# Kernel tuning notes

Measured on AMD Instinct MI355X. Metric: run time of the kernel, lower is better.

The kernel has to match this reference:

```python
import jax, jax.numpy as jnp
import numpy as np

RANK = 4
ALPHA = 32
SCALING = ALPHA / RANK  # 8.0
LORA_STRENGTH = 1.0


def setup_inputs() -> dict:
    key = jax.random.key(0)
    ks = jax.random.split(key, 7)
    d_out, d_in = 4096, 4096  # Mistral q/k/v/o_proj weight shape
    batch, seq = 1, 512
    x = jax.random.normal(ks[0], (batch, seq, d_in), dtype=jnp.float32)
    W = jax.random.normal(ks[1], (d_out, d_in), dtype=jnp.float32) * 0.02  # frozen base weight
    A = jax.random.normal(ks[2], (d_out, RANK), dtype=jnp.float32)
    B = jax.random.normal(ks[3], (RANK, d_in), dtype=jnp.float32)
    zc_w = jax.random.normal(ks[4], (), dtype=jnp.float32)  # Conv2d(1,1,1) weight (scalar)
    zc_b = jax.random.normal(ks[5], (), dtype=jnp.float32)  # Conv2d(1,1,1) bias (scalar)
    bias = jax.random.normal(ks[6], (d_out,), dtype=jnp.float32)
    return {"x": x, "W": W, "A": A, "B": B, "zc_w": zc_w, "zc_b": zc_b, "bias": bias}


def reference(x, W, A, B, zc_w, zc_b, bias):
    # low_rank_update = scaling * (A @ B), then 1x1 zero-conv = elementwise scale + bias
    low = SCALING * jnp.einsum('or,ri->oi', A, B)          # [d_out, d_in]
    low = zc_w * low + zc_b                                 # zero_conv (scalar affine)
    W_prime = LORA_STRENGTH * W + low                       # [d_out, d_in]
    # x @ W_prime.T + bias
    return jnp.einsum('bsi,oi->bso', x, W_prime) + bias
```

## Files before the change

### kernel.cpp

```cpp
#include <hip/hip_runtime.h>
#include <hip/hip_bf16.h>


typedef __attribute__((ext_vector_type(8))) short bf16x8;
typedef __attribute__((ext_vector_type(4))) short bf16x4;
typedef __attribute__((ext_vector_type(4))) unsigned short u16x4;
typedef __attribute__((ext_vector_type(4))) float f32x4;

#define MDIM 512
#define NDIM 4096
#define KDIM 4096
#define BM 128
#define BN 128
#define BK 64
#define NT (KDIM / BK)

#define VMCNT(n) asm volatile("s_waitcnt vmcnt(" #n ")" ::: "memory")
#define LGKM0()  asm volatile("s_waitcnt lgkmcnt(0)" ::: "memory")
#define SCHED0() __builtin_amdgcn_sched_barrier(0)

static __device__ inline unsigned short f2bf(float f) {
  return __bfloat16_as_ushort(__float2bfloat16(f));
}

static __device__ inline bf16x8 pack8(f32x4 a, f32x4 b) {
  bf16x8 v;
  v[0] = (short)f2bf(a[0]); v[1] = (short)f2bf(a[1]);
  v[2] = (short)f2bf(a[2]); v[3] = (short)f2bf(a[3]);
  v[4] = (short)f2bf(b[0]); v[5] = (short)f2bf(b[1]);
  v[6] = (short)f2bf(b[2]); v[7] = (short)f2bf(b[3]);
  return v;
}

static __device__ inline void gll16(const void* g, void* l) {
  __builtin_amdgcn_global_load_lds(
      (const __attribute__((address_space(1))) void*)g,
      (__attribute__((address_space(3))) void*)l, 16, 0, 0);
}

__global__ __launch_bounds__(256) void tk_kernel(
    const float* __restrict__ x, const float* __restrict__ B,
    float* __restrict__ t, float* __restrict__ xs,
    unsigned short* __restrict__ xbf) {
  const int tid = threadIdx.x;
  const int s = blockIdx.x;
  const float* xr = x + (long)s * KDIM;
  float a0 = 0.f, a1 = 0.f, a2 = 0.f, a3 = 0.f, a4 = 0.f;
  for (int k = tid * 4; k < KDIM; k += 1024) {
    f32x4 xv = *(const f32x4*)&xr[k];
    if (xbf) {
      bf16x4 bv;
      bv[0] = (short)f2bf(xv[0]); bv[1] = (short)f2bf(xv[1]);
      bv[2] = (short)f2bf(xv[2]); bv[3] = (short)f2bf(xv[3]);
      *(bf16x4*)&xbf[(long)s * KDIM + k] = bv;
    }
    f32x4 b0 = *(const f32x4*)&B[0 * KDIM + k];
    f32x4 b1 = *(const f32x4*)&B[1 * KDIM + k];
    f32x4 b2 = *(const f32x4*)&B[2 * KDIM + k];
    f32x4 b3 = *(const f32x4*)&B[3 * KDIM + k];
    a0 += xv[0]*b0[0] + xv[1]*b0[1] + xv[2]*b0[2] + xv[3]*b0[3];
    a1 += xv[0]*b1[0] + xv[1]*b1[1] + xv[2]*b1[2] + xv[3]*b1[3];
    a2 += xv[0]*b2[0] + xv[1]*b2[1] + xv[2]*b2[2] + xv[3]*b2[3];
    a3 += xv[0]*b3[0] + xv[1]*b3[1] + xv[2]*b3[2] + xv[3]*b3[3];
    a4 += xv[0] + xv[1] + xv[2] + xv[3];
  }
  #pragma unroll
  for (int off = 32; off; off >>= 1) {
    a0 += __shfl_down(a0, off, 64);
    a1 += __shfl_down(a1, off, 64);
    a2 += __shfl_down(a2, off, 64);
    a3 += __shfl_down(a3, off, 64);
    a4 += __shfl_down(a4, off, 64);
  }
  __shared__ float red[4][5];
  int w = tid >> 6, l = tid & 63;
  if (l == 0) { red[w][0]=a0; red[w][1]=a1; red[w][2]=a2; red[w][3]=a3; red[w][4]=a4; }
  __syncthreads();
  if (tid == 0) {
    t[0 * MDIM + s] = red[0][0] + red[1][0] + red[2][0] + red[3][0];
    t[1 * MDIM + s] = red[0][1] + red[1][1] + red[2][1] + red[3][1];
    t[2 * MDIM + s] = red[0][2] + red[1][2] + red[2][2] + red[3][2];
    t[3 * MDIM + s] = red[0][3] + red[1][3] + red[2][3] + red[3][3];
    xs[s]           = red[0][4] + red[1][4] + red[2][4] + red[3][4];
  }
}

template<int NSPLIT, bool FUSED>
__global__ __launch_bounds__(256) void gemm_v10(
    const unsigned short* __restrict__ xb, const float* __restrict__ W,
    const float* __restrict__ A, const float* __restrict__ bias,
    const float* __restrict__ zcw, const float* __restrict__ zcb,
    const float* __restrict__ t, const float* __restrict__ xs,
    float* __restrict__ dst) {
  __shared__ __align__(16) unsigned short As[2][BM * BK];
  __shared__ __align__(16) unsigned short Ws[2][BN * BK];

  const int bm = blockIdx.x >> 5;
  const int bn = blockIdx.x & 31;
  const int ks = blockIdx.y;
  const int NTloc = NT / NSPLIT;
  const int kbase = ks * (KDIM / NSPLIT);

  const int tid = threadIdx.x;
  const int lane = tid & 63;
  const int wv = tid >> 6;
  const int wm = wv >> 1;
  const int wn = wv & 1;

  const int srow8 = lane >> 3;
  const int schk = (lane & 7) ^ srow8;
  const unsigned short* xsrc[4];
  #pragma unroll
  for (int i = 0; i < 4; ++i)
    xsrc[i] = xb + (long)(bm * BM + i * 32 + wv * 8 + srow8) * KDIM + kbase + schk * 8;

  auto XSTAGE = [&](int kt, int slot) {
    const int koff = kt * BK;
    #pragma unroll
    for (int i = 0; i < 4; ++i)
      gll16(xsrc[i] + koff, &As[slot][i * 2048 + wv * 512]);
  };

  const int wrow = wv * 32 + (lane >> 4);
  const float* wgp = W + (long)(bn * BN + wrow) * KDIM + kbase + (lane & 15) * 4;
  const int wc = (lane & 15) >> 1;
  const int wh = (lane & 1) * 4;

  f32x4 wrA[8], wrB[8];
  auto WISSUE = [&](f32x4 (&wr)[8], int kt) {
    const float* base = wgp + kt * BK;
    #pragma unroll
    for (int i = 0; i < 8; ++i) {
      const float* p = base + (long)i * 4 * KDIM;
      asm volatile("global_load_dwordx4 %0, %1, off"
                   : "=v"(wr[i]) : "v"(p) : "memory");
    }
  };
  auto WWRITE = [&](const f32x4 (&wr)[8], int slot) {
    #pragma unroll
    for (int i = 0; i < 8; ++i) {
      const int r = wrow + i * 4;
      u16x4 v;
      v[0] = f2bf(wr[i][0]); v[1] = f2bf(wr[i][1]);
      v[2] = f2bf(wr[i][2]); v[3] = f2bf(wr[i][3]);
      *(u16x4*)&Ws[slot][r * 64 + ((wc ^ (r & 7)) << 3) + wh] = v;
    }
  };

  const int fr = lane & 15;
  const int q = lane >> 4;
  const int frs = fr & 7;

  f32x4 acc[4][4] = {};

  auto COMPUTE = [&](int slot) {
    #pragma unroll
    for (int kseg = 0; kseg < 2; ++kseg) {
      const int c = ((kseg * 4 + q) ^ frs) * 8;
      bf16x8 af[4], wf[4];
      #pragma unroll
      for (int mi = 0; mi < 4; ++mi)
        af[mi] = *(const bf16x8*)&As[slot][(wm * 64 + mi * 16 + fr) * 64 + c];
      #pragma unroll
      for (int ni = 0; ni < 4; ++ni)
        wf[ni] = *(const bf16x8*)&Ws[slot][(wn * 64 + ni * 16 + fr) * 64 + c];
      #pragma unroll
      for (int mi = 0; mi < 4; ++mi)
        #pragma unroll
        for (int ni = 0; ni < 4; ++ni)
          acc[mi][ni] = __builtin_amdgcn_mfma_f32_16x16x32_bf16(
              af[mi], wf[ni], acc[mi][ni], 0, 0, 0);
    }
  };

  WISSUE(wrA, 0);
  XSTAGE(0, 0);
  WISSUE(wrB, 1);
  VMCNT(12); SCHED0();
  WWRITE(wrA, 0);
  VMCNT(8);
  LGKM0();
  __builtin_amdgcn_s_barrier();
  SCHED0();

  auto BODY = [&](int kt, const f32x4 (&bCon)[8], f32x4 (&bFill)[8]) {
    XSTAGE(kt + 1, (kt + 1) & 1);
    WISSUE(bFill, kt + 2);
    VMCNT(12); SCHED0();
    WWRITE(bCon, (kt + 1) & 1);
    COMPUTE(kt & 1);
    VMCNT(8);
    LGKM0();
    __builtin_amdgcn_s_barrier();
    SCHED0();
  };
  for (int kt = 0; kt < NTloc - 2; kt += 2) {
    BODY(kt, wrB, wrA);
    BODY(kt + 1, wrA, wrB);
  }
  XSTAGE(NTloc - 1, (NTloc - 1) & 1);
  VMCNT(4); SCHED0();
  WWRITE(wrB, (NTloc - 1) & 1);
  COMPUTE((NTloc - 2) & 1);
  VMCNT(0);
  LGKM0();
  __builtin_amdgcn_s_barrier();
  SCHED0();
  COMPUTE((NTloc - 1) & 1);

  const int s0 = bm * BM + wm * 64;
  const int o0 = bn * BN + wn * 64;
  if (FUSED) {
    const float zw8 = zcw[0] * 8.0f;
    const float zb = zcb[0];
    #pragma unroll
    for (int mi = 0; mi < 4; ++mi) {
      const int sb = s0 + mi * 16 + q * 4;
      f32x4 t0 = *(const f32x4*)&t[0 * MDIM + sb];
      f32x4 t1 = *(const f32x4*)&t[1 * MDIM + sb];
      f32x4 t2 = *(const f32x4*)&t[2 * MDIM + sb];
      f32x4 t3 = *(const f32x4*)&t[3 * MDIM + sb];
      f32x4 x4 = *(const f32x4*)&xs[sb];
      #pragma unroll
      for (int ni = 0; ni < 4; ++ni) {
        const int o = o0 + ni * 16 + fr;
        f32x4 a4 = *(const f32x4*)&A[o * 4];
        const float bo = bias[o];
        #pragma unroll
        for (int j = 0; j < 4; ++j) {
          float corr = zw8 * (a4[0] * t0[j] + a4[1] * t1[j] + a4[2] * t2[j] + a4[3] * t3[j])
                     + zb * x4[j] + bo;
          dst[(long)(sb + j) * NDIM + o] = acc[mi][ni][j] + corr;
        }
      }
    }
  } else {
    float* p = dst + (size_t)ks * MDIM * NDIM;
    #pragma unroll
    for (int mi = 0; mi < 4; ++mi) {
      const int sb = s0 + mi * 16 + q * 4;
      #pragma unroll
      for (int ni = 0; ni < 4; ++ni) {
        const int o = o0 + ni * 16 + fr;
        #pragma unroll
        for (int j = 0; j < 4; ++j)
          p[(long)(sb + j) * NDIM + o] = acc[mi][ni][j];
      }
    }
  }
}

__global__ __launch_bounds__(256) void reduce_kernel(
    const float* __restrict__ p,
    const float* __restrict__ A, const float* __restrict__ bias,
    const float* __restrict__ zcw, const float* __restrict__ zcb,
    const float* __restrict__ t, const float* __restrict__ xs,
    float* __restrict__ out) {
  const long base = ((long)blockIdx.x * 256 + threadIdx.x) * 4;
  const int s = (int)(base / NDIM);
  const int o = (int)(base % NDIM);
  f32x4 v0 = *(const f32x4*)&p[base];
  f32x4 v1 = *(const f32x4*)&p[(long)MDIM * NDIM + base];
  f32x4 v2 = *(const f32x4*)&p[(long)2 * MDIM * NDIM + base];
  f32x4 v3 = *(const f32x4*)&p[(long)3 * MDIM * NDIM + base];
  const float zw8 = zcw[0] * 8.0f;
  const float zb = zcb[0];
  const float t0 = t[0 * MDIM + s], t1 = t[1 * MDIM + s];
  const float t2 = t[2 * MDIM + s], t3 = t[3 * MDIM + s];
  const float xv = xs[s];
  f32x4 bo = *(const f32x4*)&bias[o];
  f32x4 r;
  #pragma unroll
  for (int j = 0; j < 4; ++j) {
    f32x4 a4 = *(const f32x4*)&A[(o + j) * 4];
    r[j] = (v0[j] + v1[j]) + (v2[j] + v3[j])
         + zw8 * (a4[0] * t0 + a4[1] * t1 + a4[2] * t2 + a4[3] * t3)
         + zb * xv + bo[j];
  }
  *(f32x4*)&out[base] = r;
}

__global__ __launch_bounds__(256) void gemm_fallback(
    const float* __restrict__ x, const float* __restrict__ W,
    const float* __restrict__ A, const float* __restrict__ bias,
    const float* __restrict__ zcw, const float* __restrict__ zcb,
    const float* __restrict__ t, const float* __restrict__ xs,
    float* __restrict__ out) {
  __shared__ __align__(16) unsigned short Asf[2][64 * 64];
  __shared__ __align__(16) unsigned short Wsf[2][64 * 64];
  const int bid = blockIdx.x;
  const int bn = bid & 63, bm = bid >> 6;
  const int tid = threadIdx.x, lane = tid & 63, wid = tid >> 6;
  const int wm = wid >> 1, wn = wid & 1;
  const int srow = tid >> 2, sc0 = (tid & 3) * 16;
  const float* xg = x + (long)(bm * 64 + srow) * KDIM + sc0;
  const float* wg = W + (long)(bn * 64 + srow) * KDIM + sc0;
  const int off0 = (srow * 64 + sc0) ^ ((srow & 7) << 3);
  const int off1 = (srow * 64 + sc0 + 8) ^ ((srow & 7) << 3);
  const int fr = lane & 15, fk = (lane >> 4) * 8;
  f32x4 acc[2][2] = {};
  f32x4 xv0, xv1, xv2, xv3, wv0, wv1, wv2, wv3;
  xv0 = *(const f32x4*)(xg);      xv1 = *(const f32x4*)(xg + 4);
  xv2 = *(const f32x4*)(xg + 8);  xv3 = *(const f32x4*)(xg + 12);
  wv0 = *(const f32x4*)(wg);      wv1 = *(const f32x4*)(wg + 4);
  wv2 = *(const f32x4*)(wg + 8);  wv3 = *(const f32x4*)(wg + 12);
  *(bf16x8*)&Asf[0][off0] = pack8(xv0, xv1);
  *(bf16x8*)&Asf[0][off1] = pack8(xv2, xv3);
  *(bf16x8*)&Wsf[0][off0] = pack8(wv0, wv1);
  *(bf16x8*)&Wsf[0][off1] = pack8(wv2, wv3);
  __syncthreads();
  for (int kt = 0; kt < KDIM / 64; ++kt) {
    const int cur = kt & 1;
    if (kt + 1 < KDIM / 64) {
      const int off = (kt + 1) * 64;
      xv0 = *(const f32x4*)(xg + off);      xv1 = *(const f32x4*)(xg + off + 4);
      xv2 = *(const f32x4*)(xg + off + 8);  xv3 = *(const f32x4*)(xg + off + 12);
      wv0 = *(const f32x4*)(wg + off);      wv1 = *(const f32x4*)(wg + off + 4);
      wv2 = *(const f32x4*)(wg + off + 8);  wv3 = *(const f32x4*)(wg + off + 12);
    }
    #pragma unroll
    for (int kss = 0; kss < 2; ++kss) {
      const int kk = kss * 32 + fk;
      const int ra0 = wm * 32 + fr, ra1 = ra0 + 16;
      const int rb0 = wn * 32 + fr, rb1 = rb0 + 16;
      bf16x8 a0 = *(const bf16x8*)&Asf[cur][(ra0 * 64 + kk) ^ ((ra0 & 7) << 3)];
      bf16x8 a1 = *(const bf16x8*)&Asf[cur][(ra1 * 64 + kk) ^ ((ra1 & 7) << 3)];
      bf16x8 b0 = *(const bf16x8*)&Wsf[cur][(rb0 * 64 + kk) ^ ((rb0 & 7) << 3)];
      bf16x8 b1 = *(const bf16x8*)&Wsf[cur][(rb1 * 64 + kk) ^ ((rb1 & 7) << 3)];
      acc[0][0] = __builtin_amdgcn_mfma_f32_16x16x32_bf16(a0, b0, acc[0][0], 0, 0, 0);
      acc[0][1] = __builtin_amdgcn_mfma_f32_16x16x32_bf16(a0, b1, acc[0][1], 0, 0, 0);
      acc[1][0] = __builtin_amdgcn_mfma_f32_16x16x32_bf16(a1, b0, acc[1][0], 0, 0, 0);
      acc[1][1] = __builtin_amdgcn_mfma_f32_16x16x32_bf16(a1, b1, acc[1][1], 0, 0, 0);
    }
    if (kt + 1 < KDIM / 64) {
      const int nxt = cur ^ 1;
      *(bf16x8*)&Asf[nxt][off0] = pack8(xv0, xv1);
      *(bf16x8*)&Asf[nxt][off1] = pack8(xv2, xv3);
      *(bf16x8*)&Wsf[nxt][off0] = pack8(wv0, wv1);
      *(bf16x8*)&Wsf[nxt][off1] = pack8(wv2, wv3);
    }
    __syncthreads();
  }
  const float zw8 = zcw[0] * 8.0f;
  const float zb = zcb[0];
  const int s0 = bm * 64 + wm * 32;
  const int o0 = bn * 64 + wn * 32;
  #pragma unroll
  for (int mi = 0; mi < 2; ++mi) {
    const int sb = s0 + mi * 16 + ((lane >> 4) * 4);
    f32x4 t0 = *(const f32x4*)&t[0 * MDIM + sb];
    f32x4 t1 = *(const f32x4*)&t[1 * MDIM + sb];
    f32x4 t2 = *(const f32x4*)&t[2 * MDIM + sb];
    f32x4 t3 = *(const f32x4*)&t[3 * MDIM + sb];
    f32x4 x4 = *(const f32x4*)&xs[sb];
    #pragma unroll
    for (int ni = 0; ni < 2; ++ni) {
      const int o = o0 + ni * 16 + fr;
      f32x4 a4 = *(const f32x4*)&A[o * 4];
      const float bo = bias[o];
      #pragma unroll
      for (int j = 0; j < 4; ++j) {
        float corr = zw8 * (a4[0] * t0[j] + a4[1] * t1[j] + a4[2] * t2[j] + a4[3] * t3[j])
                   + zb * x4[j] + bo;
        out[(long)(sb + j) * NDIM + o] = acc[mi][ni][j] + corr;
      }
    }
  }
}

extern "C" void kernel_launch(void* const* d_in, const int* in_sizes, int n_in,
                              void* d_out, int out_size, void* d_ws, size_t ws_size,
                              hipStream_t stream) {
  const float* x    = (const float*)d_in[0];
  const float* W    = (const float*)d_in[1];
  const float* A    = (const float*)d_in[2];
  const float* B    = (const float*)d_in[3];
  const float* zcw  = (const float*)d_in[4];
  const float* zcb  = (const float*)d_in[5];
  const float* bias = (const float*)d_in[6];
  float* out = (float*)d_out;

  float* t  = (float*)d_ws;
  float* xs = t + 4 * MDIM;
  unsigned short* xbf = (unsigned short*)(t + 4096);
  float* pbuf = (float*)(xbf + (size_t)MDIM * KDIM);

  const size_t need_x = 4096u * 4 + (size_t)MDIM * KDIM * 2;
  const size_t need_p = need_x + (size_t)4 * MDIM * NDIM * 4;

  if (ws_size >= need_p) {
    tk_kernel<<<MDIM, 256, 0, stream>>>(x, B, t, xs, xbf);
    gemm_v10<4, false><<<dim3(4 * 32, 4), 256, 0, stream>>>(
        xbf, W, A, bias, zcw, zcb, t, xs, pbuf);
    reduce_kernel<<<(MDIM * NDIM) / (4 * 256), 256, 0, stream>>>(
        pbuf, A, bias, zcw, zcb, t, xs, out);
  } else if (ws_size >= need_x) {
    tk_kernel<<<MDIM, 256, 0, stream>>>(x, B, t, xs, xbf);
    gemm_v10<1, true><<<dim3(4 * 32, 1), 256, 0, stream>>>(
        xbf, W, A, bias, zcw, zcb, t, xs, out);
  } else {
    tk_kernel<<<MDIM, 256, 0, stream>>>(x, B, t, xs, nullptr);
    gemm_fallback<<<(MDIM / 64) * (NDIM / 64), 256, 0, stream>>>(
        x, W, A, bias, zcw, zcb, t, xs, out);
  }
}
```

Measured before the change: 46.09 us.

## Triple-buffer X tiles in LDS and raise wave priority around MFMA block

The bf16 activation tile in shared memory goes from a double buffer to a triple buffer. X is now staged two k-steps ahead, and the second wait on outstanding global loads inside each iteration is dropped, so loads overlap more with compute. The MFMA section is also wrapped in s_setprio to favour issuing the matrix ops. This uses more LDS, which may reduce occupancy, and the reworked vmcnt accounting could race if the load counts do not line up.

```diff
diff --git a/kernel.cpp b/kernel.cpp
--- a/kernel.cpp
+++ b/kernel.cpp
@@ -86,13 +86,13 @@
 }
 
 template<int NSPLIT, bool FUSED>
-__global__ __launch_bounds__(256) void gemm_v10(
+__global__ __launch_bounds__(256) void gemm_v11(
     const unsigned short* __restrict__ xb, const float* __restrict__ W,
     const float* __restrict__ A, const float* __restrict__ bias,
     const float* __restrict__ zcw, const float* __restrict__ zcb,
     const float* __restrict__ t, const float* __restrict__ xs,
     float* __restrict__ dst) {
-  __shared__ __align__(16) unsigned short As[2][BM * BK];
+  __shared__ __align__(16) unsigned short As[3][BM * BK];
   __shared__ __align__(16) unsigned short Ws[2][BN * BK];
 
   const int bm = blockIdx.x >> 5;
@@ -153,60 +153,63 @@
 
   f32x4 acc[4][4] = {};
 
-  auto COMPUTE = [&](int slot) {
+  auto COMPUTE = [&](int xslot, int wslot) {
     #pragma unroll
     for (int kseg = 0; kseg < 2; ++kseg) {
       const int c = ((kseg * 4 + q) ^ frs) * 8;
       bf16x8 af[4], wf[4];
       #pragma unroll
       for (int mi = 0; mi < 4; ++mi)
-        af[mi] = *(const bf16x8*)&As[slot][(wm * 64 + mi * 16 + fr) * 64 + c];
+        af[mi] = *(const bf16x8*)&As[xslot][(wm * 64 + mi * 16 + fr) * 64 + c];
       #pragma unroll
       for (int ni = 0; ni < 4; ++ni)
-        wf[ni] = *(const bf16x8*)&Ws[slot][(wn * 64 + ni * 16 + fr) * 64 + c];
+        wf[ni] = *(const bf16x8*)&Ws[wslot][(wn * 64 + ni * 16 + fr) * 64 + c];
+      __builtin_amdgcn_s_setprio(1);
       #pragma unroll
       for (int mi = 0; mi < 4; ++mi)
         #pragma unroll
         for (int ni = 0; ni < 4; ++ni)
           acc[mi][ni] = __builtin_amdgcn_mfma_f32_16x16x32_bf16(
               af[mi], wf[ni], acc[mi][ni], 0, 0, 0);
+      __builtin_amdgcn_s_setprio(0);
     }
   };
 
   WISSUE(wrA, 0);
   XSTAGE(0, 0);
+  XSTAGE(1, 1);
   WISSUE(wrB, 1);
+  VMCNT(16); SCHED0();
+  WWRITE(wrA, 0);
   VMCNT(12); SCHED0();
-  WWRITE(wrA, 0);
-  VMCNT(8);
   LGKM0();
   __builtin_amdgcn_s_barrier();
   SCHED0();
 
-  auto BODY = [&](int kt, const f32x4 (&bCon)[8], f32x4 (&bFill)[8]) {
-    XSTAGE(kt + 1, (kt + 1) & 1);
-    WISSUE(bFill, kt + 2);
-    VMCNT(12); SCHED0();
-    WWRITE(bCon, (kt + 1) & 1);
-    COMPUTE(kt & 1);
-    VMCNT(8);
-    LGKM0();
-    __builtin_amdgcn_s_barrier();
-    SCHED0();
-  };
+  #define BODY(KT, BFILL, BCON)                                   \
+    do {                                                          \
+      XSTAGE((KT) + 2, ((KT) + 2) % 3);             \
+      WISSUE(BFILL, (KT) + 2);                      \
+      VMCNT(12); SCHED0();                \
+      WWRITE(BCON, ((KT) + 1) & 1);                               \
+      COMPUTE((KT) % 3, (KT) & 1);                                \
+      LGKM0();                                                    \
+      __builtin_amdgcn_s_barrier();                               \
+      SCHED0();                                                   \
+    } while (0)
+
   for (int kt = 0; kt < NTloc - 2; kt += 2) {
-    BODY(kt, wrB, wrA);
-    BODY(kt + 1, wrA, wrB);
-  }
-  XSTAGE(NTloc - 1, (NTloc - 1) & 1);
-  VMCNT(4); SCHED0();
+    BODY(kt, wrA, wrB);
+    BODY(kt + 1, wrB, wrA);
+  }
+  #undef BODY
+  VMCNT(0); SCHED0();
   WWRITE(wrB, (NTloc - 1) & 1);
-  COMPUTE((NTloc - 2) & 1);
-  VMCNT(0);
+  COMPUTE((NTloc - 2) % 3, (NTloc - 2) & 1);
   LGKM0();
   __builtin_amdgcn_s_barrier();
   SCHED0();
-  COMPUTE((NTloc - 1) & 1);
+  COMPUTE((NTloc - 1) % 3, (NTloc - 1) & 1);
 
   const int s0 = bm * BM + wm * 64;
   const int o0 = bn * BN + wn * 64;
@@ -390,13 +393,13 @@
 
   if (ws_size >= need_p) {
     tk_kernel<<<MDIM, 256, 0, stream>>>(x, B, t, xs, xbf);
-    gemm_v10<4, false><<<dim3(4 * 32, 4), 256, 0, stream>>>(
+    gemm_v11<4, false><<<dim3(4 * 32, 4), 256, 0, stream>>>(
         xbf, W, A, bias, zcw, zcb, t, xs, pbuf);
     reduce_kernel<<<(MDIM * NDIM) / (4 * 256), 256, 0, stream>>>(
         pbuf, A, bias, zcw, zcb, t, xs, out);
   } else if (ws_size >= need_x) {
     tk_kernel<<<MDIM, 256, 0, stream>>>(x, B, t, xs, xbf);
-    gemm_v10<1, true><<<dim3(4 * 32, 1), 256, 0, stream>>>(
+    gemm_v11<1, true><<<dim3(4 * 32, 1), 256, 0, stream>>>(
         xbf, W, A, bias, zcw, zcb, t, xs, out);
   } else {
     tk_kernel<<<MDIM, 256, 0, stream>>>(x, B, t, xs, nullptr);
```

After: 46.64 us. No clear change (+1.2%).
